# Kernel optimization log

Hardware: AMD Instinct MI355X
Metric: run time of the kernel (lower is better)

Reference implementation:

```python
import jax, jax.numpy as jnp
import numpy as np

INPUT_DIM, HIDDEN, CB_DIM, CB_SIZE = 768, 512, 256, 512
COMMIT_W = 1.0


def setup_inputs() -> dict:
    key = jax.random.key(0)
    ks = jax.random.split(key, 10)
    def lin(k, fan_in, fan_out):
        lim = 1.0 / np.sqrt(fan_in)
        return jax.random.uniform(k, (fan_in, fan_out), jnp.float32, -lim, lim)
    return {
        "x": jax.random.normal(ks[0], (32, 2048, INPUT_DIM), jnp.float32),
        "W1": lin(ks[1], INPUT_DIM, HIDDEN),
        "b1": jnp.zeros((HIDDEN,), jnp.float32),
        "W2": lin(ks[2], HIDDEN, CB_DIM),
        "b2": jnp.zeros((CB_DIM,), jnp.float32),
        "codebook": jax.random.normal(ks[3], (CB_SIZE, CB_DIM), jnp.float32),
        "W3": lin(ks[4], CB_DIM, HIDDEN),
        "b3": jnp.zeros((HIDDEN,), jnp.float32),
        "W4": lin(ks[5], HIDDEN, INPUT_DIM),
        "b4": jnp.zeros((INPUT_DIM,), jnp.float32),
    }


def reference(x, W1, b1, W2, b2, codebook, W3, b3, W4, b4):
    # encoder MLP: [b, n, 768] -> [b, n, 256]
    h = jax.nn.relu(jnp.einsum('bnd,dh->bnh', x, W1) + b1)
    z = jnp.einsum('bnh,hc->bnc', h, W2) + b2

    # VQ: squared-L2 distance to codebook, argmin, gather
    # d(z, c) = ||z||^2 - 2 z.c + ||c||^2  (||z||^2 constant over argmin, omitted)
    dots = jnp.einsum('bnc,kc->bnk', z, codebook)          # [b, n, K]
    c_sq = jnp.sum(codebook * codebook, axis=-1)            # [K]
    indices = jnp.argmin(c_sq - 2.0 * dots, axis=-1)        # [b, n] int
    q = codebook[indices]                                   # [b, n, 256] gather

    # straight-through estimator + commitment loss
    quantized = z + jax.lax.stop_gradient(q - z)
    commit_loss = COMMIT_W * jnp.mean((z - jax.lax.stop_gradient(q)) ** 2)

    # decoder MLP: [b, n, 256] -> [b, n, 768]
    h2 = jax.nn.relu(jnp.einsum('bnc,ch->bnh', quantized, W3) + b3)
    recon = jnp.einsum('bnh,hd->bnd', h2, W4) + b4
    return recon, indices.astype(jnp.int32), commit_loss
```

## Files before the change

### kernel.cpp

```cpp
#include <hip/hip_runtime.h>

typedef unsigned short u16;
typedef unsigned int   u32;
typedef __attribute__((ext_vector_type(8))) short short8;
typedef __attribute__((ext_vector_type(4))) float f32x4;

#define NTOK 65536
#define IND  768
#define HID  512
#define CBD  256
#define CBS  512

#define OUT_IDX_OFF   ((size_t)NTOK * IND)
#define OUT_LOSS_OFF  (OUT_IDX_OFF + NTOK)

#define OFF_H      ((size_t)0)
#define OFF_Z      ((size_t)134217728)
#define OFF_W1H    ((size_t)201326592)
#define OFF_W1L    ((size_t)202113024)
#define OFF_W2H    ((size_t)202899456)
#define OFF_W2L    ((size_t)203161600)
#define OFF_CBH    ((size_t)203423744)
#define OFF_CBL    ((size_t)203685888)
#define OFF_CSQ    ((size_t)203948032)
#define OFF_PART   ((size_t)0)
#define OFF_TABLE  ((size_t)8388608)
#define OFF_ZSQ    ((size_t)9961472)
#define OFF_IDX    ((size_t)10223616)
#define OFF_FLAGS  ((size_t)10485760)
#define OFF_CNT    ((size_t)10747904)
#define OFF_HFIX   ((size_t)16777216)
#define OFF_ZFIX   ((size_t)83886080)
#define FCHUNK 32768

__device__ __forceinline__ u16 f2bf(float f) {
    u32 u = __float_as_uint(f);
    return (u16)((u + 0x7fffu + ((u >> 16) & 1u)) >> 16);
}
__device__ __forceinline__ float bf2f(u16 h) {
    return __uint_as_float(((u32)h) << 16);
}

__global__ __launch_bounds__(256) void cbsplit(
    const float* __restrict__ cb, u16* __restrict__ hi, u16* __restrict__ lo,
    float* __restrict__ csq)
{
    int c = blockIdx.x, t = threadIdx.x;
    float v = cb[(size_t)c * CBD + t];
    u16 h = f2bf(v); u16 l = f2bf(v - bf2f(h));
    hi[(size_t)c * CBD + t] = h; lo[(size_t)c * CBD + t] = l;
    __shared__ float red[256];
    red[t] = v * v; __syncthreads();
    for (int s = 128; s; s >>= 1) { if (t < s) red[t] += red[t + s]; __syncthreads(); }
    if (!t) csq[c] = red[0];
}

__global__ __launch_bounds__(256) void wsplit(
    const float* __restrict__ W, u16* __restrict__ hi, u16* __restrict__ lo,
    int K, int N)
{
    int n = blockIdx.x;
    for (int k = threadIdx.x; k < K; k += 256) {
        float v = W[(size_t)k * N + n];
        u16 h = f2bf(v); u16 l = f2bf(v - bf2f(h));
        hi[(size_t)n * K + k] = h; lo[(size_t)n * K + k] = l;
    }
}

#define CHS 1040
#define PLN (4 * CHS)

template<int AMODE, int EPI>
__global__ __launch_bounds__(256, 2) void gemm3(
    const float* __restrict__ Af, const u32* __restrict__ Apk,
    const u16* __restrict__ Bhi, const u16* __restrict__ Blo,
    const float* __restrict__ bias,
    u32* __restrict__ Opk, float* __restrict__ Opart,
    int M, int N, int K)
{
    __shared__ u16 lds[4 * PLN];
    u16* sAh = lds;
    u16* sAl = lds + PLN;
    u16* sBh = lds + 2 * PLN;
    u16* sBl = lds + 3 * PLN;
    const int tid  = threadIdx.x;

    const int nwg = gridDim.x * gridDim.y;
    const int hw  = blockIdx.y * gridDim.x + blockIdx.x;
    const int logical = (hw & 7) * (nwg >> 3) + (hw >> 3);
    const int bx = logical % gridDim.x;
    const int by = logical / gridDim.x;

    const int m0 = by * 128, n0 = bx * 128;
    const int w = tid >> 6, lane = tid & 63, quad = lane >> 4, l15 = lane & 15;
    const int wm = (w & 1) * 64, wn = (w >> 1) * 64;

    f32x4 acc[4][4] = {};

    for (int k0 = 0; k0 < K; k0 += 32) {
        __syncthreads();
        if (AMODE == 0) {
            #pragma unroll
            for (int s = 0; s < 4; ++s) {
                int slot = tid + s * 256;
                int m = slot >> 3, kg = (slot & 7) << 2;
                int c = kg >> 3, off = kg & 7;
                float4 v = *(const float4*)(Af + (size_t)(m0 + m) * K + k0 + kg);
                u16 h0 = f2bf(v.x), h1 = f2bf(v.y), h2 = f2bf(v.z), h3 = f2bf(v.w);
                ushort4 hv = {h0, h1, h2, h3};
                ushort4 lv = {f2bf(v.x - bf2f(h0)), f2bf(v.y - bf2f(h1)),
                              f2bf(v.z - bf2f(h2)), f2bf(v.w - bf2f(h3))};
                *(ushort4*)&sAh[c * CHS + m * 8 + off] = hv;
                *(ushort4*)&sAl[c * CHS + m * 8 + off] = lv;
            }
        } else {
            #pragma unroll
            for (int s = 0; s < 4; ++s) {
                int slot = tid + s * 256;
                int m = slot >> 3, ke = (slot & 7) << 2;
                int c = ke >> 3, off = ke & 7;
                uint4 u = *(const uint4*)(Apk + (size_t)(m0 + m) * K + k0 + ke);
                ushort4 hv = {(u16)(u.x & 0xffff), (u16)(u.y & 0xffff),
                              (u16)(u.z & 0xffff), (u16)(u.w & 0xffff)};
                ushort4 lv = {(u16)(u.x >> 16), (u16)(u.y >> 16),
                              (u16)(u.z >> 16), (u16)(u.w >> 16)};
                *(ushort4*)&sAh[c * CHS + m * 8 + off] = hv;
                *(ushort4*)&sAl[c * CHS + m * 8 + off] = lv;
            }
        }
        #pragma unroll
        for (int s = 0; s < 4; ++s) {
            int slot = tid + s * 256;
            int n = (slot & 511) >> 2, ku = slot & 3;
            const u16* src = (slot < 512) ? Bhi : Blo;
            u16* dst = (slot < 512) ? sBh : sBl;
            uint4 u = *(const uint4*)(src + (size_t)(n0 + n) * K + k0 + ku * 8);
            *(uint4*)&dst[ku * CHS + n * 8] = u;
        }
        __syncthreads();

        short8 ah[4], al[4], bh[4], bl[4];
        const int kc = quad * CHS;
        #pragma unroll
        for (int i = 0; i < 4; ++i) {
            int ar = wm + i * 16 + l15;
            int br = wn + i * 16 + l15;
            ah[i] = *(const short8*)&sAh[kc + ar * 8];
            al[i] = *(const short8*)&sAl[kc + ar * 8];
            bh[i] = *(const short8*)&sBh[kc + br * 8];
            bl[i] = *(const short8*)&sBl[kc + br * 8];
        }
        #pragma unroll
        for (int i = 0; i < 4; ++i)
            #pragma unroll
            for (int j = 0; j < 4; ++j) {
                acc[i][j] = __builtin_amdgcn_mfma_f32_16x16x32_bf16(ah[i], bh[j], acc[i][j], 0, 0, 0);
                acc[i][j] = __builtin_amdgcn_mfma_f32_16x16x32_bf16(ah[i], bl[j], acc[i][j], 0, 0, 0);
                acc[i][j] = __builtin_amdgcn_mfma_f32_16x16x32_bf16(al[i], bh[j], acc[i][j], 0, 0, 0);
            }
    }

    if (EPI <= 1) {
        float bn[4];
        #pragma unroll
        for (int j = 0; j < 4; ++j) bn[j] = bias[n0 + wn + j * 16 + l15];
        #pragma unroll
        for (int i = 0; i < 4; ++i)
            #pragma unroll
            for (int r = 0; r < 4; ++r) {
                int row = m0 + wm + i * 16 + quad * 4 + r;
                #pragma unroll
                for (int j = 0; j < 4; ++j) {
                    float v = acc[i][j][r] + bn[j];
                    if (EPI == 0) v = fmaxf(v, 0.f);
                    u16 h = f2bf(v); u16 l = f2bf(v - bf2f(h));
                    Opk[(size_t)row * N + n0 + wn + j * 16 + l15] = (u32)h | ((u32)l << 16);
                }
            }
    } else {
        float cs[4]; int cidx[4];
        #pragma unroll
        for (int j = 0; j < 4; ++j) {
            cidx[j] = n0 + wn + j * 16 + l15;
            cs[j] = bias[cidx[j]];
        }
        const int nparts = gridDim.x * 2;
        const int pslot  = bx * 2 + (w >> 1);
        #pragma unroll
        for (int i = 0; i < 4; ++i)
            #pragma unroll
            for (int r = 0; r < 4; ++r) {
                int row = m0 + wm + i * 16 + quad * 4 + r;
                float d1 = 3.4e38f, d2 = 3.4e38f; int i1 = 0x7fffffff;
                #pragma unroll
                for (int j = 0; j < 4; ++j) {
                    float v = fmaf(-2.0f, acc[i][j][r], cs[j]);
                    if (v < d1) { d2 = d1; d1 = v; i1 = cidx[j]; }
                    else d2 = fminf(d2, v);
                }
                #pragma unroll
                for (int mm = 1; mm < 16; mm <<= 1) {
                    float od1 = __shfl_xor(d1, mm, 64);
                    float od2 = __shfl_xor(d2, mm, 64);
                    int   oi1 = __shfl_xor(i1, mm, 64);
                    if (od1 < d1 || (od1 == d1 && oi1 < i1)) { d2 = fminf(d1, od2); d1 = od1; i1 = oi1; }
                    else d2 = fminf(d2, od1);
                }
                if (l15 == 0) {
                    float4 o = {d1, d2, __int_as_float(i1), 0.f};
                    *(float4*)&Opart[((size_t)row * nparts + pslot) * 4] = o;
                }
            }
    }
}

__global__ __launch_bounds__(256) void zsq_pk(
    const u32* __restrict__ Zpk, float* __restrict__ zsq)
{
    int tok = blockIdx.x * 4 + (threadIdx.x >> 6);
    int lane = threadIdx.x & 63;
    uint4 u = *(const uint4*)(Zpk + (size_t)tok * CBD + lane * 4);
    float z0 = bf2f((u16)(u.x & 0xffff)) + bf2f((u16)(u.x >> 16));
    float z1 = bf2f((u16)(u.y & 0xffff)) + bf2f((u16)(u.y >> 16));
    float z2 = bf2f((u16)(u.z & 0xffff)) + bf2f((u16)(u.z >> 16));
    float z3 = bf2f((u16)(u.w & 0xffff)) + bf2f((u16)(u.w >> 16));
    float s = z0 * z0 + z1 * z1 + z2 * z2 + z3 * z3;
    #pragma unroll
    for (int off = 32; off; off >>= 1) s += __shfl_down(s, off, 64);
    if (!lane) zsq[tok] = s;
}

__global__ __launch_bounds__(256) void vq_reduce(
    const float* __restrict__ part, const float* __restrict__ zsq,
    float* __restrict__ out_idx, int* __restrict__ idx_i,
    int* __restrict__ cnt, float* __restrict__ accum, int* __restrict__ flags)
{
    int tok = blockIdx.x * 256 + threadIdx.x;
    float d1 = 3.4e38f, d2 = 3.4e38f; int i1 = 0x7fffffff;
    #pragma unroll
    for (int nb = 0; nb < 8; ++nb) {
        float4 p = *(const float4*)&part[((size_t)tok * 8 + nb) * 4];
        float pd1 = p.x, pd2 = p.y; int pi1 = __float_as_int(p.z);
        if (pd1 < d1 || (pd1 == d1 && pi1 < i1)) { d2 = fminf(d1, pd2); d1 = pd1; i1 = pi1; }
        else d2 = fminf(d2, pd1);
    }
    out_idx[tok] = (float)i1;
    idx_i[tok] = i1;
    if (d2 - d1 < 0.01f) {
        int p = atomicAdd(cnt, 1);
        if (p >= 0 && p < NTOK) flags[p] = tok;
    }
    float c = zsq[tok] + d1;
    __shared__ float red[256];
    red[threadIdx.x] = c; __syncthreads();
    for (int s = 128; s; s >>= 1) { if (threadIdx.x < s) red[threadIdx.x] += red[threadIdx.x + s]; __syncthreads(); }
    if (!threadIdx.x) atomicAdd(accum, red[0]);
}

__device__ __forceinline__ void fma16(float (&a)[4][4],
    float x0, float x1, float x2, float x3, float4 w)
{
    a[0][0] = fmaf(x0, w.x, a[0][0]); a[0][1] = fmaf(x0, w.y, a[0][1]);
    a[0][2] = fmaf(x0, w.z, a[0][2]); a[0][3] = fmaf(x0, w.w, a[0][3]);
    a[1][0] = fmaf(x1, w.x, a[1][0]); a[1][1] = fmaf(x1, w.y, a[1][1]);
    a[1][2] = fmaf(x1, w.z, a[1][2]); a[1][3] = fmaf(x1, w.w, a[1][3]);
    a[2][0] = fmaf(x2, w.x, a[2][0]); a[2][1] = fmaf(x2, w.y, a[2][1]);
    a[2][2] = fmaf(x2, w.z, a[2][2]); a[2][3] = fmaf(x2, w.w, a[2][3]);
    a[3][0] = fmaf(x3, w.x, a[3][0]); a[3][1] = fmaf(x3, w.y, a[3][1]);
    a[3][2] = fmaf(x3, w.z, a[3][2]); a[3][3] = fmaf(x3, w.w, a[3][3]);
}

template<int K, int N, int RELU, int MODE>
__global__ __launch_bounds__(256) void fixup_gemm(
    const int* __restrict__ cnt, const int* __restrict__ flags, int base,
    const float* __restrict__ A, const float* __restrict__ W,
    const float* __restrict__ bias, float* __restrict__ C)
{
    __shared__ float xs[64][68];
    __shared__ float Wt[64][68];
    __shared__ int   tok_s[64];
    int n = cnt[0]; if (n > NTOK) n = NTOK;
    int nc = n - base; if (nc <= 0) return; if (nc > FCHUNK) nc = FCHUNK;
    const int ntile = (nc + 63) >> 6;
    const int items = ntile * (N >> 6);
    const int t = threadIdx.x;
    const int tg4 = (t >> 4) << 2;
    const int cg  = t & 15;

    for (int it = blockIdx.x; it < items; it += gridDim.x) {
        const int tt = it / (N >> 6);
        const int ct = it - tt * (N >> 6);
        const int j0 = ct * 64;
        const int trow = tt * 64;
        __syncthreads();
        if (MODE == 0 && t < 64) {
            int fi = base + trow + t; if (fi > n - 1) fi = n - 1;
            tok_s[t] = flags[fi];
        }
        __syncthreads();

        float a[4][4];
        float4 bb = *(const float4*)(bias + j0 + cg * 4);
        #pragma unroll
        for (int ti = 0; ti < 4; ++ti) {
            a[ti][0] = bb.x; a[ti][1] = bb.y; a[ti][2] = bb.z; a[ti][3] = bb.w;
        }

        for (int k0 = 0; k0 < K; k0 += 64) {
            __syncthreads();
            #pragma unroll
            for (int s = 0; s < 4; ++s) {
                int slot = t + s * 256;
                int row = slot >> 4, c4 = slot & 15;
                const float* src = (MODE == 0)
                    ? A + (size_t)tok_s[row] * K + k0 + c4 * 4
                    : A + (size_t)(trow + row) * K + k0 + c4 * 4;
                *(float4*)&xs[row][c4 * 4] = *(const float4*)src;
            }
            #pragma unroll
            for (int s = 0; s < 4; ++s) {
                int slot = t + s * 256;
                int kk = slot >> 4, c4 = slot & 15;
                *(float4*)&Wt[kk][c4 * 4] =
                    *(const float4*)(W + (size_t)(k0 + kk) * N + j0 + c4 * 4);
            }
            __syncthreads();
            #pragma unroll 4
            for (int k4 = 0; k4 < 16; ++k4) {
                float4 xv0 = *(const float4*)&xs[tg4 + 0][k4 * 4];
                float4 xv1 = *(const float4*)&xs[tg4 + 1][k4 * 4];
                float4 xv2 = *(const float4*)&xs[tg4 + 2][k4 * 4];
                float4 xv3 = *(const float4*)&xs[tg4 + 3][k4 * 4];
                float4 w0 = *(const float4*)&Wt[k4 * 4 + 0][cg * 4];
                float4 w1 = *(const float4*)&Wt[k4 * 4 + 1][cg * 4];
                float4 w2 = *(const float4*)&Wt[k4 * 4 + 2][cg * 4];
                float4 w3 = *(const float4*)&Wt[k4 * 4 + 3][cg * 4];
                fma16(a, xv0.x, xv1.x, xv2.x, xv3.x, w0);
                fma16(a, xv0.y, xv1.y, xv2.y, xv3.y, w1);
                fma16(a, xv0.z, xv1.z, xv2.z, xv3.z, w2);
                fma16(a, xv0.w, xv1.w, xv2.w, xv3.w, w3);
            }
        }
        #pragma unroll
        for (int ti = 0; ti < 4; ++ti) {
            float4 o;
            if (RELU) {
                o.x = fmaxf(a[ti][0], 0.f); o.y = fmaxf(a[ti][1], 0.f);
                o.z = fmaxf(a[ti][2], 0.f); o.w = fmaxf(a[ti][3], 0.f);
            } else {
                o.x = a[ti][0]; o.y = a[ti][1]; o.z = a[ti][2]; o.w = a[ti][3];
            }
            *(float4*)&C[(size_t)(trow + tg4 + ti) * N + j0 + cg * 4] = o;
        }
    }
}

__global__ __launch_bounds__(256) void fixup_d(
    const int* __restrict__ cnt, const int* __restrict__ flags, int base,
    const float* __restrict__ zbuf, const float* __restrict__ cb,
    const float* __restrict__ csq,
    int* __restrict__ idx_i, float* __restrict__ out_idx)
{
    __shared__ float zs[32][CBD];
    __shared__ float csq_s[CBS];
    __shared__ float bd_s[4][8];
    __shared__ int   bi_s[4][8];
    int n = cnt[0]; if (n > NTOK) n = NTOK;
    int nc = n - base; if (nc <= 0) return; if (nc > FCHUNK) nc = FCHUNK;
    const int ntile = (nc + 31) >> 5;
    const int t = threadIdx.x;
    const int wv = t >> 6, l = t & 63;
    if (t < 128) *(float4*)&csq_s[t * 4] = *(const float4*)(csq + t * 4);

    for (int it = blockIdx.x; it < ntile; it += gridDim.x) {
        __syncthreads();
        #pragma unroll
        for (int s = 0; s < 8; ++s) {
            int slot = t + s * 256;
            int row = slot >> 6, c4 = slot & 63;
            *(float4*)&zs[row][c4 * 4] =
                *(const float4*)(zbuf + (size_t)(it * 32 + row) * CBD + c4 * 4);
        }
        __syncthreads();
        for (int sb = 0; sb < 4; ++sb) {
            const float* cb0 = cb + (size_t)t * CBD;
            const float* cb1 = cb + (size_t)(t + 256) * CBD;
            float d0[8], d1[8];
            #pragma unroll
            for (int tt = 0; tt < 8; ++tt) { d0[tt] = 0.f; d1[tt] = 0.f; }
            float4 pA = *(const float4*)(cb0);
            float4 pB = *(const float4*)(cb1);
            for (int k4 = 0; k4 < 64; ++k4) {
                float4 cA = pA, cB = pB;
                int kn = (k4 + 1 < 64) ? (k4 + 1) : 63;
                pA = *(const float4*)(cb0 + kn * 4);
                pB = *(const float4*)(cb1 + kn * 4);
                #pragma unroll
                for (int tt = 0; tt < 8; ++tt) {
                    float4 zv = *(const float4*)&zs[sb * 8 + tt][k4 * 4];
                    d0[tt] = fmaf(zv.w, cA.w, fmaf(zv.z, cA.z,
                             fmaf(zv.y, cA.y, fmaf(zv.x, cA.x, d0[tt]))));
                    d1[tt] = fmaf(zv.w, cB.w, fmaf(zv.z, cB.z,
                             fmaf(zv.y, cB.y, fmaf(zv.x, cB.x, d1[tt]))));
                }
            }
            float bd[8]; int bi[8];
            const float cs0 = csq_s[t], cs1 = csq_s[t + 256];
            #pragma unroll
            for (int tt = 0; tt < 8; ++tt) {
                float e0 = cs0 - 2.f * d0[tt];
                float e1 = cs1 - 2.f * d1[tt];
                if (e0 <= e1) { bd[tt] = e0; bi[tt] = t; }
                else          { bd[tt] = e1; bi[tt] = t + 256; }
            }
            #pragma unroll
            for (int mm = 1; mm < 64; mm <<= 1) {
                #pragma unroll
                for (int tt = 0; tt < 8; ++tt) {
                    float od = __shfl_xor(bd[tt], mm, 64);
                    int   oi = __shfl_xor(bi[tt], mm, 64);
                    if (od < bd[tt] || (od == bd[tt] && oi < bi[tt])) { bd[tt] = od; bi[tt] = oi; }
                }
            }
            if (l == 0) {
                #pragma unroll
                for (int tt = 0; tt < 8; ++tt) { bd_s[wv][tt] = bd[tt]; bi_s[wv][tt] = bi[tt]; }
            }
            __syncthreads();
            if (t < 8) {
                const int tt = t;
                float d = bd_s[0][tt]; int i = bi_s[0][tt];
                #pragma unroll
                for (int v2 = 1; v2 < 4; ++v2) {
                    float od = bd_s[v2][tt]; int oi = bi_s[v2][tt];
                    if (od < d || (od == d && oi < i)) { d = od; i = oi; }
                }
                int fi = base + it * 32 + sb * 8 + tt;
                if (fi < n) {
                    int tok = flags[fi];
                    idx_i[tok] = i; out_idx[tok] = (float)i;
                }
            }
            __syncthreads();
        }
    }
}

__global__ __launch_bounds__(256) void table_pre(
    const float* __restrict__ cb, const float* __restrict__ W3,
    const float* __restrict__ b3, const float* __restrict__ W4,
    const float* __restrict__ b4, float* __restrict__ table)
{
    __shared__ float crow[CBD];
    __shared__ float h2[HID];
    const int c = blockIdx.x;
    const int t = threadIdx.x;
    crow[t] = cb[(size_t)c * CBD + t];
    __syncthreads();
    #pragma unroll
    for (int s = 0; s < 2; ++s) {
        int j = t + s * 256;
        float acc = b3[j];
        for (int k = 0; k < CBD; ++k) acc = fmaf(crow[k], W3[(size_t)k * HID + j], acc);
        h2[j] = fmaxf(acc, 0.f);
    }
    __syncthreads();
    #pragma unroll
    for (int s = 0; s < 3; ++s) {
        int j = t + s * 256;
        float acc = b4[j];
        for (int k = 0; k < HID; ++k) acc = fmaf(h2[k], W4[(size_t)k * IND + j], acc);
        table[(size_t)c * IND + j] = acc;
    }
}

__global__ __launch_bounds__(256) void gather_kernel(
    const int* __restrict__ idx, const float* __restrict__ table,
    float* __restrict__ out)
{
    unsigned i = blockIdx.x * 256u + threadIdx.x;
    unsigned tok = i / 192u;
    unsigned c = i - tok * 192u;
    int id = idx[tok];
    ((float4*)out)[i] = ((const float4*)table)[(size_t)id * 192 + c];
}

__global__ void finalize_kernel(const float* __restrict__ accum,
                                float* __restrict__ out_loss)
{
    out_loss[0] = accum[0] * (1.0f / 16777216.0f);
}

extern "C" void kernel_launch(void* const* d_in, const int* in_sizes, int n_in,
                              void* d_out, int out_size, void* d_ws, size_t ws_size,
                              hipStream_t stream) {
    const float* x  = (const float*)d_in[0];
    const float* W1 = (const float*)d_in[1];
    const float* b1 = (const float*)d_in[2];
    const float* W2 = (const float*)d_in[3];
    const float* b2 = (const float*)d_in[4];
    const float* cb = (const float*)d_in[5];
    const float* W3 = (const float*)d_in[6];
    const float* b3 = (const float*)d_in[7];
    const float* W4 = (const float*)d_in[8];
    const float* b4 = (const float*)d_in[9];

    char* ws = (char*)d_ws;
    u32*  Hpk   = (u32*)(ws + OFF_H);
    u32*  Zpk   = (u32*)(ws + OFF_Z);
    u16*  W1h   = (u16*)(ws + OFF_W1H);
    u16*  W1l   = (u16*)(ws + OFF_W1L);
    u16*  W2h   = (u16*)(ws + OFF_W2H);
    u16*  W2l   = (u16*)(ws + OFF_W2L);
    u16*  CBh   = (u16*)(ws + OFF_CBH);
    u16*  CBl   = (u16*)(ws + OFF_CBL);
    float* csq  = (float*)(ws + OFF_CSQ);
    float* part = (float*)(ws + OFF_PART);
    float* table = (float*)(ws + OFF_TABLE);
    float* zsq  = (float*)(ws + OFF_ZSQ);
    int*   idx_i = (int*)(ws + OFF_IDX);
    int*   flags = (int*)(ws + OFF_FLAGS);
    int*   cnt   = (int*)(ws + OFF_CNT);
    float* accum = (float*)(ws + OFF_CNT + 4);
    float* hfix  = (float*)(ws + OFF_HFIX);
    float* zfix  = (float*)(ws + OFF_ZFIX);

    float* out      = (float*)d_out;
    float* out_idx  = out + OUT_IDX_OFF;
    float* out_loss = out + OUT_LOSS_OFF;

    cbsplit<<<CBS, 256, 0, stream>>>(cb, CBh, CBl, csq);
    wsplit<<<HID, 256, 0, stream>>>(W1, W1h, W1l, IND, HID);
    wsplit<<<CBD, 256, 0, stream>>>(W2, W2h, W2l, HID, CBD);

    gemm3<0, 0><<<dim3(HID / 128, NTOK / 128), 256, 0, stream>>>(
        x, (const u32*)nullptr, W1h, W1l, b1, Hpk, (float*)nullptr, NTOK, HID, IND);
    gemm3<1, 1><<<dim3(CBD / 128, NTOK / 128), 256, 0, stream>>>(
        (const float*)nullptr, Hpk, W2h, W2l, b2, Zpk, (float*)nullptr, NTOK, CBD, HID);

    hipMemsetAsync(cnt, 0, 8, stream);

    zsq_pk<<<NTOK / 4, 256, 0, stream>>>(Zpk, zsq);

    gemm3<1, 2><<<dim3(CBS / 128, NTOK / 128), 256, 0, stream>>>(
        (const float*)nullptr, Zpk, CBh, CBl, csq, (u32*)nullptr, part, NTOK, CBS, CBD);

    table_pre<<<CBS, 256, 0, stream>>>(cb, W3, b3, W4, b4, table);

    vq_reduce<<<NTOK / 256, 256, 0, stream>>>(part, zsq, out_idx, idx_i, cnt, accum, flags);

    for (int pass = 0; pass < 2; ++pass) {
        int base = pass * FCHUNK;
        fixup_gemm<IND, HID, 1, 0><<<1024, 256, 0, stream>>>(
            cnt, flags, base, x, W1, b1, hfix);
        fixup_gemm<HID, CBD, 0, 1><<<512, 256, 0, stream>>>(
            cnt, flags, base, hfix, W2, b2, zfix);
        fixup_d<<<512, 256, 0, stream>>>(
            cnt, flags, base, zfix, cb, csq, idx_i, out_idx);
    }

    gather_kernel<<<(NTOK * (IND / 4)) / 256, 256, 0, stream>>>(idx_i, table, out);

    finalize_kernel<<<1, 1, 0, stream>>>(accum, out_loss);
}
```

Measured before the change: 875.6 us.

## Split packed hi/lo activations into planes and load tiles via direct global-to-LDS DMA

Intermediate activations H and Z are now stored as separate hi and lo bf16 planes instead of packed u32 words. The GEMM B operand (and the A operand when already bf16) is loaded with global_load_lds 16-byte DMA into an XOR-swizzled LDS layout. This replaces register-staged loads and unpacking, aiming to cut VGPR traffic and LDS bank conflicts in the K loop. It adds a new swizzle scheme and two half-width stores per epilogue element, with a risk of layout or synchronisation mistakes around the DMA writes.

Result: faster. 851.3 us (-2.8%).

```diff
diff --git a/kernel.cpp b/kernel.cpp
--- a/kernel.cpp
+++ b/kernel.cpp
@@ -14,8 +14,10 @@
 #define OUT_IDX_OFF   ((size_t)NTOK * IND)
 #define OUT_LOSS_OFF  (OUT_IDX_OFF + NTOK)
 
-#define OFF_H      ((size_t)0)
-#define OFF_Z      ((size_t)134217728)
+#define OFF_HH     ((size_t)0)
+#define OFF_HL     ((size_t)67108864)
+#define OFF_ZH     ((size_t)134217728)
+#define OFF_ZL     ((size_t)167772160)
 #define OFF_W1H    ((size_t)201326592)
 #define OFF_W1L    ((size_t)202113024)
 #define OFF_W2H    ((size_t)202899456)
@@ -41,6 +43,12 @@
     return __uint_as_float(((u32)h) << 16);
 }
 
+__device__ __forceinline__ void dma16(const void* g, void* l) {
+    __builtin_amdgcn_global_load_lds(
+        (const __attribute__((address_space(1))) u32*)g,
+        (__attribute__((address_space(3))) u32*)l, 16, 0, 0);
+}
+
 __global__ __launch_bounds__(256) void cbsplit(
     const float* __restrict__ cb, u16* __restrict__ hi, u16* __restrict__ lo,
     float* __restrict__ csq)
@@ -68,21 +76,22 @@
 }
 
 #define CHS 1040
-#define PLN (4 * CHS)
 
 template<int AMODE, int EPI>
 __global__ __launch_bounds__(256, 2) void gemm3(
-    const float* __restrict__ Af, const u32* __restrict__ Apk,
+    const float* __restrict__ Af,
+    const u16* __restrict__ Ahi, const u16* __restrict__ Alo,
     const u16* __restrict__ Bhi, const u16* __restrict__ Blo,
     const float* __restrict__ bias,
-    u32* __restrict__ Opk, float* __restrict__ Opart,
+    u16* __restrict__ Ohi, u16* __restrict__ Olo, float* __restrict__ Opart,
     int M, int N, int K)
 {
-    __shared__ u16 lds[4 * PLN];
+    constexpr int APL = (AMODE == 0) ? 4160 : 4096;
+    __shared__ u16 lds[2 * 4160 + 2 * 4096];
     u16* sAh = lds;
-    u16* sAl = lds + PLN;
-    u16* sBh = lds + 2 * PLN;
-    u16* sBl = lds + 3 * PLN;
+    u16* sAl = lds + APL;
+    u16* sBh = lds + 2 * APL;
+    u16* sBl = lds + 2 * APL + 4096;
     const int tid  = threadIdx.x;
 
     const int nwg = gridDim.x * gridDim.y;
@@ -94,12 +103,32 @@
     const int m0 = by * 128, n0 = bx * 128;
     const int w = tid >> 6, lane = tid & 63, quad = lane >> 4, l15 = lane & 15;
     const int wm = (w & 1) * 64, wn = (w >> 1) * 64;
+    const int dmarow = lane >> 2;
+    const int dmaq   = (lane & 3) ^ ((lane >> 3) & 3);
+    const int fx     = (quad ^ ((l15 >> 1) & 3)) << 3;
 
     f32x4 acc[4][4] = {};
 
     for (int k0 = 0; k0 < K; k0 += 32) {
         __syncthreads();
-        if (AMODE == 0) {
+        #pragma unroll
+        for (int g = 0; g < 4; ++g) {
+            int wl = w * 4 + g;
+            int r0 = (wl & 7) << 4;
+            const u16* P = (wl & 8) ? Blo : Bhi;
+            u16* D = ((wl & 8) ? sBl : sBh) + r0 * 32;
+            dma16(P + (size_t)(n0 + r0 + dmarow) * K + k0 + dmaq * 8, D);
+        }
+        if (AMODE == 1) {
+            #pragma unroll
+            for (int g = 0; g < 4; ++g) {
+                int wl = w * 4 + g;
+                int r0 = (wl & 7) << 4;
+                const u16* P = (wl & 8) ? Alo : Ahi;
+                u16* D = ((wl & 8) ? sAl : sAh) + r0 * 32;
+                dma16(P + (size_t)(m0 + r0 + dmarow) * K + k0 + dmaq * 8, D);
+            }
+        } else {
             #pragma unroll
             for (int s = 0; s < 4; ++s) {
                 int slot = tid + s * 256;
@@ -113,42 +142,23 @@
                 *(ushort4*)&sAh[c * CHS + m * 8 + off] = hv;
                 *(ushort4*)&sAl[c * CHS + m * 8 + off] = lv;
             }
-        } else {
-            #pragma unroll
-            for (int s = 0; s < 4; ++s) {
-                int slot = tid + s * 256;
-                int m = slot >> 3, ke = (slot & 7) << 2;
-                int c = ke >> 3, off = ke & 7;
-                uint4 u = *(const uint4*)(Apk + (size_t)(m0 + m) * K + k0 + ke);
-                ushort4 hv = {(u16)(u.x & 0xffff), (u16)(u.y & 0xffff),
-                              (u16)(u.z & 0xffff), (u16)(u.w & 0xffff)};
-                ushort4 lv = {(u16)(u.x >> 16), (u16)(u.y >> 16),
-                              (u16)(u.z >> 16), (u16)(u.w >> 16)};
-                *(ushort4*)&sAh[c * CHS + m * 8 + off] = hv;
-                *(ushort4*)&sAl[c * CHS + m * 8 + off] = lv;
-            }
-        }
-        #pragma unroll
-        for (int s = 0; s < 4; ++s) {
-            int slot = tid + s * 256;
-            int n = (slot & 511) >> 2, ku = slot & 3;
-            const u16* src = (slot < 512) ? Bhi : Blo;
-            u16* dst = (slot < 512) ? sBh : sBl;
-            uint4 u = *(const uint4*)(src + (size_t)(n0 + n) * K + k0 + ku * 8);
-            *(uint4*)&dst[ku * CHS + n * 8] = u;
         }
         __syncthreads();
 
         short8 ah[4], al[4], bh[4], bl[4];
-        const int kc = quad * CHS;
         #pragma unroll
         for (int i = 0; i < 4; ++i) {
             int ar = wm + i * 16 + l15;
             int br = wn + i * 16 + l15;
-            ah[i] = *(const short8*)&sAh[kc + ar * 8];
-            al[i] = *(const short8*)&sAl[kc + ar * 8];
-            bh[i] = *(const short8*)&sBh[kc + br * 8];
-            bl[i] = *(const short8*)&sBl[kc + br * 8];
+            if (AMODE == 0) {
+                ah[i] = *(const short8*)&sAh[quad * CHS + ar * 8];
+                al[i] = *(const short8*)&sAl[quad * CHS + ar * 8];
+            } else {
+                ah[i] = *(const short8*)&sAh[ar * 32 + fx];
+                al[i] = *(const short8*)&sAl[ar * 32 + fx];
+            }
+            bh[i] = *(const short8*)&sBh[br * 32 + fx];
+            bl[i] = *(const short8*)&sBl[br * 32 + fx];
         }
         #pragma unroll
         for (int i = 0; i < 4; ++i)
@@ -174,7 +184,8 @@
                     float v = acc[i][j][r] + bn[j];
                     if (EPI == 0) v = fmaxf(v, 0.f);
                     u16 h = f2bf(v); u16 l = f2bf(v - bf2f(h));
-                    Opk[(size_t)row * N + n0 + wn + j * 16 + l15] = (u32)h | ((u32)l << 16);
+                    size_t o = (size_t)row * N + n0 + wn + j * 16 + l15;
+                    Ohi[o] = h; Olo[o] = l;
                 }
             }
     } else {
@@ -215,15 +226,16 @@
 }
 
 __global__ __launch_bounds__(256) void zsq_pk(
-    const u32* __restrict__ Zpk, float* __restrict__ zsq)
+    const u16* __restrict__ Zh, const u16* __restrict__ Zl, float* __restrict__ zsq)
 {
     int tok = blockIdx.x * 4 + (threadIdx.x >> 6);
     int lane = threadIdx.x & 63;
-    uint4 u = *(const uint4*)(Zpk + (size_t)tok * CBD + lane * 4);
-    float z0 = bf2f((u16)(u.x & 0xffff)) + bf2f((u16)(u.x >> 16));
-    float z1 = bf2f((u16)(u.y & 0xffff)) + bf2f((u16)(u.y >> 16));
-    float z2 = bf2f((u16)(u.z & 0xffff)) + bf2f((u16)(u.z >> 16));
-    float z3 = bf2f((u16)(u.w & 0xffff)) + bf2f((u16)(u.w >> 16));
+    ushort4 uh = *(const ushort4*)(Zh + (size_t)tok * CBD + lane * 4);
+    ushort4 ul = *(const ushort4*)(Zl + (size_t)tok * CBD + lane * 4);
+    float z0 = bf2f(uh.x) + bf2f(ul.x);
+    float z1 = bf2f(uh.y) + bf2f(ul.y);
+    float z2 = bf2f(uh.z) + bf2f(ul.z);
+    float z3 = bf2f(uh.w) + bf2f(ul.w);
     float s = z0 * z0 + z1 * z1 + z2 * z2 + z3 * z3;
     #pragma unroll
     for (int off = 32; off; off >>= 1) s += __shfl_down(s, off, 64);
@@ -506,8 +518,10 @@
     const float* b4 = (const float*)d_in[9];
 
     char* ws = (char*)d_ws;
-    u32*  Hpk   = (u32*)(ws + OFF_H);
-    u32*  Zpk   = (u32*)(ws + OFF_Z);
+    u16*  Hh    = (u16*)(ws + OFF_HH);
+    u16*  Hl    = (u16*)(ws + OFF_HL);
+    u16*  Zh    = (u16*)(ws + OFF_ZH);
+    u16*  Zl    = (u16*)(ws + OFF_ZL);
     u16*  W1h   = (u16*)(ws + OFF_W1H);
     u16*  W1l   = (u16*)(ws + OFF_W1L);
     u16*  W2h   = (u16*)(ws + OFF_W2H);
@@ -534,16 +548,19 @@
     wsplit<<<CBD, 256, 0, stream>>>(W2, W2h, W2l, HID, CBD);
 
     gemm3<0, 0><<<dim3(HID / 128, NTOK / 128), 256, 0, stream>>>(
-        x, (const u32*)nullptr, W1h, W1l, b1, Hpk, (float*)nullptr, NTOK, HID, IND);
+        x, (const u16*)nullptr, (const u16*)nullptr, W1h, W1l, b1,
+        Hh, Hl, (float*)nullptr, NTOK, HID, IND);
     gemm3<1, 1><<<dim3(CBD / 128, NTOK / 128), 256, 0, stream>>>(
-        (const float*)nullptr, Hpk, W2h, W2l, b2, Zpk, (float*)nullptr, NTOK, CBD, HID);
+        (const float*)nullptr, Hh, Hl, W2h, W2l, b2,
+        Zh, Zl, (float*)nullptr, NTOK, CBD, HID);
 
     hipMemsetAsync(cnt, 0, 8, stream);
 
-    zsq_pk<<<NTOK / 4, 256, 0, stream>>>(Zpk, zsq);
+    zsq_pk<<<NTOK / 4, 256, 0, stream>>>(Zh, Zl, zsq);
 
     gemm3<1, 2><<<dim3(CBS / 128, NTOK / 128), 256, 0, stream>>>(
-        (const float*)nullptr, Zpk, CBh, CBl, csq, (u32*)nullptr, part, NTOK, CBS, CBD);
+        (const float*)nullptr, Zh, Zl, CBh, CBl, csq,
+        (u16*)nullptr, (u16*)nullptr, part, NTOK, CBS, CBD);
 
     table_pre<<<CBS, 256, 0, stream>>>(cb, W3, b3, W4, b4, table);
 
```
